# Optimization experiments

Measured on AMD Instinct MI355X. Metric: run time of the kernel, lower is better.

## Reference

```python
import jax, jax.numpy as jnp
import numpy as np
from jax import lax


def _na_indices(size, k):
    # NATTEN-style window: window shifts to stay inside the volume.
    centers = np.arange(size)
    start = np.clip(centers - k // 2, 0, size - k)
    idx = start[:, None] + np.arange(k)[None, :]          # (size, k) neighbor coords
    rel = idx - centers[:, None] + (k - 1)                # (size, k) in [0, 2k-2]
    return jnp.asarray(idx), jnp.asarray(rel)


def _ln(x, g, b):
    mu = jnp.mean(x, axis=-1, keepdims=True)
    var = jnp.mean(jnp.square(x - mu), axis=-1, keepdims=True)
    return (x - mu) * lax.rsqrt(var + 1e-5) * g + b


def setup_inputs() -> dict:
    key = jax.random.key(0)
    ks = jax.random.split(key, 12)
    B, C, H, W, Z = 1, 128, 64, 64, 8
    heads, k = 8, 3
    s = lambda kk, shp: (jax.random.normal(kk, shp, jnp.float32) * 0.02)
    return {
        "x": jax.random.normal(ks[0], (B, C, H, W, Z), jnp.float32),
        "ln1_g": jnp.ones((C,), jnp.float32), "ln1_b": jnp.zeros((C,), jnp.float32),
        "qkv_w": s(ks[1], (C, 3 * C)), "qkv_b": jnp.zeros((3 * C,), jnp.float32),
        "proj_w": s(ks[2], (C, C)), "proj_b": jnp.zeros((C,), jnp.float32),
        "rpb": s(ks[3], (heads, 2 * k - 1, 2 * k - 1, 2 * k - 1)),
        "ln2_g": jnp.ones((C,), jnp.float32), "ln2_b": jnp.zeros((C,), jnp.float32),
        "w1": s(ks[4], (C, 4 * C)), "b1": jnp.zeros((4 * C,), jnp.float32),
        "w2": s(ks[5], (4 * C, C)), "b2": jnp.zeros((C,), jnp.float32),
    }


def reference(x, ln1_g, ln1_b, qkv_w, qkv_b, proj_w, proj_b, rpb,
              ln2_g, ln2_b, w1, b1, w2, b2):
    B, C, H, W, Z = x.shape
    heads = rpb.shape[0]
    k = (rpb.shape[1] + 1) // 2
    hd = C // heads
    K3 = k * k * k

    xp = jnp.transpose(x, (0, 2, 3, 4, 1))                 # (B,H,W,Z,C)
    res1 = xp
    xn = _ln(xp, ln1_g, ln1_b)
    qkv = xn @ qkv_w + qkv_b
    q, kk, v = jnp.split(qkv, 3, axis=-1)

    ih, rh = _na_indices(H, k)
    iw, rw = _na_indices(W, k)
    iz, rz = _na_indices(Z, k)
    Ih = ih[:, None, None, :, None, None]
    Iw = iw[None, :, None, None, :, None]
    Iz = iz[None, None, :, None, None, :]
    # gathered neighborhoods: (B,H,W,Z,k,k,k,C) -> (B,H,W,Z,K3,heads,hd)
    k_n = kk[:, Ih, Iw, Iz, :].reshape(B, H, W, Z, K3, heads, hd)
    v_n = v[:, Ih, Iw, Iz, :].reshape(B, H, W, Z, K3, heads, hd)
    qh = q.reshape(B, H, W, Z, heads, hd) * (hd ** -0.5)

    # scores: (B,H,W,Z,heads,K3)
    scores = jnp.einsum('bxyzne,bxyzmne->bxyznm', qh, k_n)
    bias = rpb[:, rh[:, None, None, :, None, None],
                  rw[None, :, None, None, :, None],
                  rz[None, None, :, None, None, :]]        # (heads,H,W,Z,k,k,k)
    bias = bias.reshape(heads, H, W, Z, K3).transpose(1, 2, 3, 0, 4)
    attn = jax.nn.softmax(scores + bias[None], axis=-1)

    out = jnp.einsum('bxyznm,bxyzmne->bxyzne', attn, v_n).reshape(B, H, W, Z, C)
    out = out @ proj_w + proj_b
    x1 = res1 + out                                        # attention residual
    h = jax.nn.gelu(_ln(x1, ln2_g, ln2_b) @ w1 + b1) @ w2 + b2
    x2 = x1 + h                                            # FFN residual

    enc = jnp.transpose(x2, (0, 4, 1, 2, 3))               # (B,C,H,W,Z)
    skip = enc + x                                         # outer residual
    pooled = lax.reduce_window(skip, -jnp.inf, lax.max,
                               (1, 1, 2, 2, 2), (1, 1, 2, 2, 2), 'VALID')
    return (pooled, skip)
```

## Files before the change

### kernel.cpp

```cpp
#include <hip/hip_runtime.h>
#include <hip/hip_bf16.h>
#include <math.h>

#define NPOS 32768

typedef __hip_bfloat16 bf16;
typedef __attribute__((ext_vector_type(8))) short bf16x8;
typedef __attribute__((ext_vector_type(4))) float f32x4;

__device__ __forceinline__ float bf2f(short s) {
    union { unsigned u; float f; } cv;
    cv.u = ((unsigned)(unsigned short)s) << 16;
    return cv.f;
}

__global__ __launch_bounds__(256) void prep_weights_kernel(
    const float* __restrict__ qkv_w, const float* __restrict__ proj_w,
    const float* __restrict__ w1, const float* __restrict__ w2,
    bf16* __restrict__ wt_qkv, bf16* __restrict__ wt_proj,
    bf16* __restrict__ wt_w1, bf16* __restrict__ wt_w2)
{
    int bi = blockIdx.x;
    const float* src; bf16* dst; int K, M, t;
    if (bi < 48)       { src = qkv_w;  dst = wt_qkv;  K = 128; M = 384; t = bi; }
    else if (bi < 64)  { src = proj_w; dst = wt_proj; K = 128; M = 128; t = bi - 48; }
    else if (bi < 128) { src = w1;     dst = wt_w1;   K = 128; M = 512; t = bi - 64; }
    else               { src = w2;     dst = wt_w2;   K = 512; M = 128; t = bi - 128; }
    int tiles_x = M >> 5;
    int m0 = (t % tiles_x) * 32, k0 = (t / tiles_x) * 32;
    __shared__ float tile[32][33];
    int tx = threadIdx.x & 31, ty = threadIdx.x >> 5;
    #pragma unroll
    for (int i = 0; i < 4; i++)
        tile[ty + i * 8][tx] = src[(size_t)(k0 + ty + i * 8) * M + m0 + tx];
    __syncthreads();
    #pragma unroll
    for (int i = 0; i < 4; i++)
        dst[(size_t)(m0 + ty + i * 8) * K + k0 + tx] = __float2bfloat16(tile[tx][ty + i * 8]);
}

__global__ __launch_bounds__(256) void ln1_transpose_kernel(
    const float* __restrict__ x, const float* __restrict__ g,
    const float* __restrict__ b, bf16* __restrict__ out)
{
    __shared__ float tile[128][65];
    __shared__ float red[2][64][4];
    __shared__ float smu[64], srs[64];
    int n0 = blockIdx.x * 64;
    int tid = threadIdx.x;
    #pragma unroll
    for (int i = 0; i < 32; i++) {
        int idx = i * 256 + tid;
        int c = idx >> 6, nn = idx & 63;
        tile[c][nn] = x[(size_t)c * NPOS + n0 + nn];
    }
    __syncthreads();
    {
        int p = tid >> 2, s = tid & 3;
        float sum = 0.f, ssq = 0.f;
        #pragma unroll
        for (int i = 0; i < 32; i++) {
            float v = tile[s * 32 + i][p];
            sum += v; ssq += v * v;
        }
        red[0][p][s] = sum; red[1][p][s] = ssq;
    }
    __syncthreads();
    if (tid < 64) {
        float s = red[0][tid][0] + red[0][tid][1] + red[0][tid][2] + red[0][tid][3];
        float q = red[1][tid][0] + red[1][tid][1] + red[1][tid][2] + red[1][tid][3];
        float mu = s * (1.f / 128.f);
        float var = q * (1.f / 128.f) - mu * mu;
        smu[tid] = mu;
        srs[tid] = rsqrtf(var + 1e-5f);
    }
    __syncthreads();
    #pragma unroll
    for (int i = 0; i < 32; i++) {
        int idx = i * 256 + tid;
        int nn = idx >> 7, c = idx & 127;
        out[(size_t)(n0 + nn) * 128 + c] =
            __float2bfloat16((tile[c][nn] - smu[nn]) * srs[nn] * g[c] + b[c]);
    }
}

__device__ __forceinline__ float gelu_f(float v) {
    float t = tanhf(0.7978845608028654f * (v + 0.044715f * v * v * v));
    return 0.5f * v * (1.f + t);
}

template<int MODE>
__global__ __launch_bounds__(256) void gemm_mfma_kernel(
    const bf16* __restrict__ A, const bf16* __restrict__ Bt,
    const float* __restrict__ bias, float* __restrict__ outf, bf16* __restrict__ outb,
    const float* __restrict__ aux0, const float* __restrict__ aux1,
    const float* __restrict__ lng, const float* __restrict__ lnb,
    int N, int K, int M)
{
    __shared__ __align__(16) char smem[69632];
    bf16 (*As)[136] = (bf16(*)[136])smem;
    bf16 (*Bs)[136] = (bf16(*)[136])(smem + 34816);

    int tid = threadIdx.x;
    int row0 = blockIdx.x * 128;
    int col0 = blockIdx.y * 128;
    int lane = tid & 63, wid = tid >> 6;
    int wr = wid >> 1, wc = wid & 1;
    int lr = lane & 15, kg = lane >> 4;

    f32x4 acc[4][4] = {};

    for (int k0 = 0; k0 < K; k0 += 128) {
        bf16x8 ra[8], rb[8];
        #pragma unroll
        for (int i = 0; i < 8; i++) {
            int q = i * 256 + tid;
            int r = q >> 4, c16 = q & 15;
            ra[i] = *(const bf16x8*)(A  + (size_t)(row0 + r) * K + k0 + c16 * 8);
            rb[i] = *(const bf16x8*)(Bt + (size_t)(col0 + r) * K + k0 + c16 * 8);
        }
        if (k0 > 0) __syncthreads();
        #pragma unroll
        for (int i = 0; i < 8; i++) {
            int q = i * 256 + tid;
            int r = q >> 4, c16 = q & 15;
            *(bf16x8*)&As[r][c16 * 8] = ra[i];
            *(bf16x8*)&Bs[r][c16 * 8] = rb[i];
        }
        __syncthreads();
        #pragma unroll
        for (int ks = 0; ks < 4; ks++) {
            bf16x8 af[4], bf_[4];
            #pragma unroll
            for (int m = 0; m < 4; m++)
                af[m] = *(const bf16x8*)&As[wr * 64 + m * 16 + lr][ks * 32 + kg * 8];
            #pragma unroll
            for (int n = 0; n < 4; n++)
                bf_[n] = *(const bf16x8*)&Bs[wc * 64 + n * 16 + lr][ks * 32 + kg * 8];
            #pragma unroll
            for (int m = 0; m < 4; m++)
                #pragma unroll
                for (int n = 0; n < 4; n++)
                    acc[m][n] = __builtin_amdgcn_mfma_f32_16x16x32_bf16(af[m], bf_[n], acc[m][n], 0, 0, 0);
        }
    }

    if (MODE == 0 || MODE == 2 || MODE == 3) {
        #pragma unroll
        for (int m = 0; m < 4; m++) {
            #pragma unroll
            for (int n = 0; n < 4; n++) {
                int c = col0 + wc * 64 + n * 16 + lr;
                float bv = bias[c];
                #pragma unroll
                for (int j = 0; j < 4; j++) {
                    int r = row0 + wr * 64 + m * 16 + kg * 4 + j;
                    float v = acc[m][n][j] + bv;
                    if (MODE == 0) {
                        outb[(size_t)r * M + c] = __float2bfloat16(v);
                    } else if (MODE == 2) {
                        outb[(size_t)r * M + c] = __float2bfloat16(gelu_f(v));
                    } else {
                        v += aux1[(size_t)r * 128 + c] + aux0[(size_t)c * N + r];
                        outf[(size_t)c * N + r] = v;
                    }
                }
            }
        }
    } else {
        __syncthreads();
        float (*rsum)[33] = (float(*)[33])smem;
        float (*rsq)[33]  = (float(*)[33])(smem + 16896);
        float* smu = (float*)(smem + 33792);
        float* srs = (float*)(smem + 34304);
        int slot = wc * 16 + lr;
        #pragma unroll
        for (int m = 0; m < 4; m++) {
            #pragma unroll
            for (int j = 0; j < 4; j++) {
                int rloc = wr * 64 + m * 16 + kg * 4 + j;
                int r = row0 + rloc;
                float ps = 0.f, pq = 0.f;
                #pragma unroll
                for (int n = 0; n < 4; n++) {
                    int c = wc * 64 + n * 16 + lr;
                    float v = acc[m][n][j] + bias[c] + aux0[(size_t)c * N + r];
                    acc[m][n][j] = v;
                    outf[(size_t)r * 128 + c] = v;
                    ps += v; pq += v * v;
                }
                rsum[rloc][slot] = ps;
                rsq[rloc][slot]  = pq;
            }
        }
        __syncthreads();
        if (tid < 128) {
            float s = 0.f, q = 0.f;
            #pragma unroll
            for (int i = 0; i < 32; i++) { s += rsum[tid][i]; q += rsq[tid][i]; }
            float mu = s * (1.f / 128.f);
            float var = q * (1.f / 128.f) - mu * mu;
            smu[tid] = mu;
            srs[tid] = rsqrtf(var + 1e-5f);
        }
        __syncthreads();
        #pragma unroll
        for (int m = 0; m < 4; m++) {
            #pragma unroll
            for (int j = 0; j < 4; j++) {
                int rloc = wr * 64 + m * 16 + kg * 4 + j;
                int r = row0 + rloc;
                float mu = smu[rloc], rs = srs[rloc];
                #pragma unroll
                for (int n = 0; n < 4; n++) {
                    int c = wc * 64 + n * 16 + lr;
                    float v = (acc[m][n][j] - mu) * rs * lng[c] + lnb[c];
                    outb[(size_t)r * 128 + c] = __float2bfloat16(v);
                }
            }
        }
    }
}

__global__ __launch_bounds__(256) void attn_kernel(
    const bf16* __restrict__ qkv,
    const float* __restrict__ rpb,
    bf16* __restrict__ out)
{
    int t = blockIdx.x * 256 + threadIdx.x;
    int head = t & 7, n = t >> 3;
    int z = n & 7, w = (n >> 3) & 63, h = n >> 9;

    int sh = min(max(h - 1, 0), 61);
    int sw = min(max(w - 1, 0), 61);
    int sz = min(max(z - 1, 0), 5);

    float qf[16];
    {
        const bf16* qp = qkv + (size_t)n * 384 + head * 16;
        bf16x8 q0 = *(const bf16x8*)qp;
        bf16x8 q1 = *(const bf16x8*)(qp + 8);
        #pragma unroll
        for (int e = 0; e < 8; e++) {
            qf[e]     = bf2f(q0[e]) * 0.25f;
            qf[e + 8] = bf2f(q1[e]) * 0.25f;
        }
    }

    const bf16*  kbase = qkv + (size_t)((sh << 9) + (sw << 3) + sz) * 384 + 128 + head * 16;
    const float* rp    = rpb + head * 125 + (sh - h + 2) * 25 + (sw - w + 2) * 5 + (sz - z + 2);

    float sc[27];
    float mx = -1e30f;
    #pragma unroll
    for (int a = 0; a < 3; a++) {
        #pragma unroll
        for (int b = 0; b < 3; b++) {
            #pragma unroll
            for (int c = 0; c < 3; c++) {
                const bf16* kp = kbase + (size_t)(a * 512 + b * 8 + c) * 384;
                bf16x8 k0 = *(const bf16x8*)kp;
                bf16x8 k1 = *(const bf16x8*)(kp + 8);
                float s = 0.f;
                #pragma unroll
                for (int e = 0; e < 8; e++) s = fmaf(qf[e], bf2f(k0[e]), s);
                #pragma unroll
                for (int e = 0; e < 8; e++) s = fmaf(qf[e + 8], bf2f(k1[e]), s);
                s += rp[a * 25 + b * 5 + c];
                sc[a * 9 + b * 3 + c] = s;
                mx = fmaxf(mx, s);
            }
        }
    }

    float sum = 0.f;
    #pragma unroll
    for (int m = 0; m < 27; m++) {
        float e = __expf(sc[m] - mx);
        sc[m] = e;
        sum += e;
    }
    float inv = 1.f / sum;

    float o[16] = {};
    #pragma unroll
    for (int a = 0; a < 3; a++) {
        #pragma unroll
        for (int b = 0; b < 3; b++) {
            #pragma unroll
            for (int c = 0; c < 3; c++) {
                const bf16* vp = kbase + (size_t)(a * 512 + b * 8 + c) * 384 + 128;
                bf16x8 v0 = *(const bf16x8*)vp;
                bf16x8 v1 = *(const bf16x8*)(vp + 8);
                float pm = sc[a * 9 + b * 3 + c];
                #pragma unroll
                for (int e = 0; e < 8; e++) {
                    o[e]     = fmaf(pm, bf2f(v0[e]), o[e]);
                    o[e + 8] = fmaf(pm, bf2f(v1[e]), o[e + 8]);
                }
            }
        }
    }

    short os[16];
    #pragma unroll
    for (int e = 0; e < 16; e++) {
        union { bf16 b; short s; } cv;
        cv.b = __float2bfloat16(o[e] * inv);
        os[e] = cv.s;
    }
    bf16* op = out + (size_t)n * 128 + head * 16;
    *(bf16x8*)op       = *(bf16x8*)os;
    *(bf16x8*)(op + 8) = *(bf16x8*)(os + 8);
}

__global__ __launch_bounds__(256) void pool_kernel(
    const float* __restrict__ skip, float* __restrict__ pooled)
{
    int t = blockIdx.x * 256 + threadIdx.x;
    if (t >= 128 * 32 * 32 * 4) return;
    int oz = t & 3, ow = (t >> 2) & 31, oh = (t >> 7) & 31, c = t >> 12;
    const float* base = skip + (size_t)c * 32768 + (oh * 2) * 512 + (ow * 2) * 8 + oz * 2;
    float m = -INFINITY;
    #pragma unroll
    for (int dh = 0; dh < 2; dh++)
        #pragma unroll
        for (int dw = 0; dw < 2; dw++)
            #pragma unroll
            for (int dz = 0; dz < 2; dz++)
                m = fmaxf(m, base[dh * 512 + dw * 8 + dz]);
    pooled[t] = m;
}

extern "C" void kernel_launch(void* const* d_in, const int* in_sizes, int n_in,
                              void* d_out, int out_size, void* d_ws, size_t ws_size,
                              hipStream_t stream) {
    const float* x      = (const float*)d_in[0];
    const float* ln1_g  = (const float*)d_in[1];
    const float* ln1_b  = (const float*)d_in[2];
    const float* qkv_w  = (const float*)d_in[3];
    const float* qkv_b  = (const float*)d_in[4];
    const float* proj_w = (const float*)d_in[5];
    const float* proj_b = (const float*)d_in[6];
    const float* rpb    = (const float*)d_in[7];
    const float* ln2_g  = (const float*)d_in[8];
    const float* ln2_b  = (const float*)d_in[9];
    const float* w1     = (const float*)d_in[10];
    const float* b1     = (const float*)d_in[11];
    const float* w2     = (const float*)d_in[12];
    const float* b2     = (const float*)d_in[13];

    const int N = NPOS;
    char* wsc = (char*)d_ws;
    bf16*  buf0 = (bf16*)wsc;
    bf16*  buf1 = (bf16*)(wsc + (size_t)N * 128 * 2);
    float* buf2 = (float*)(wsc + (size_t)N * 128 * 2 + (size_t)N * 512 * 2);
    char*  wts  = wsc + (size_t)N * 128 * 2 + (size_t)N * 512 * 2 + (size_t)N * 128 * 4;
    bf16* wt_qkv  = (bf16*)wts;
    bf16* wt_proj = wt_qkv  + 384 * 128;
    bf16* wt_w1   = wt_proj + 128 * 128;
    bf16* wt_w2   = wt_w1   + 512 * 128;

    float* out_pooled = (float*)d_out;
    float* out_skip   = (float*)d_out + 524288;

    prep_weights_kernel<<<192, 256, 0, stream>>>(qkv_w, proj_w, w1, w2,
                                                 wt_qkv, wt_proj, wt_w1, wt_w2);

    ln1_transpose_kernel<<<N / 64, 256, 0, stream>>>(x, ln1_g, ln1_b, buf0);

    gemm_mfma_kernel<0><<<dim3(N / 128, 3), 256, 0, stream>>>(
        buf0, wt_qkv, qkv_b, nullptr, buf1, nullptr, nullptr, nullptr, nullptr, N, 128, 384);

    attn_kernel<<<(N * 8) / 256, 256, 0, stream>>>(buf1, rpb, buf0);

    gemm_mfma_kernel<4><<<dim3(N / 128, 1), 256, 0, stream>>>(
        buf0, wt_proj, proj_b, buf2, buf0, x, nullptr, ln2_g, ln2_b, N, 128, 128);

    gemm_mfma_kernel<2><<<dim3(N / 128, 4), 256, 0, stream>>>(
        buf0, wt_w1, b1, nullptr, buf1, nullptr, nullptr, nullptr, nullptr, N, 128, 512);

    gemm_mfma_kernel<3><<<dim3(N / 128, 1), 256, 0, stream>>>(
        buf1, wt_w2, b2, out_skip, nullptr, x, buf2, nullptr, nullptr, N, 512, 128);

    pool_kernel<<<(524288 + 255) / 256, 256, 0, stream>>>(out_skip, out_pooled);
}
```

Measured before the change: 209.1 us.

## Drop LDS staging in GEMMs, load MFMA fragments directly, shrink row tiles

The GEMM kernel no longer stages A and B tiles through shared memory. Each wave loads its MFMA fragments straight from global memory, and the K loop is fully unrolled through a compile-time K template. The projection and W2 GEMMs now use 64-row tiles, which doubles their block count and improves occupancy. GELU is rewritten as a sigmoid form using __expf instead of tanhf. The direct loads give up LDS reuse across waves, so global and L2 traffic go up, and register pressure rises from the fully unrolled loop.

Result: no change. 209.6 us (+0.2%).

```diff
diff --git a/kernel.cpp b/kernel.cpp
--- a/kernel.cpp
+++ b/kernel.cpp
@@ -85,76 +85,57 @@
 }
 
 __device__ __forceinline__ float gelu_f(float v) {
-    float t = tanhf(0.7978845608028654f * (v + 0.044715f * v * v * v));
-    return 0.5f * v * (1.f + t);
-}
-
-template<int MODE>
+    float u = 0.7978845608028654f * (v + 0.044715f * v * v * v);
+    return v / (1.f + __expf(-2.f * u));
+}
+
+template<int MODE, int BM, int KT>
 __global__ __launch_bounds__(256) void gemm_mfma_kernel(
     const bf16* __restrict__ A, const bf16* __restrict__ Bt,
     const float* __restrict__ bias, float* __restrict__ outf, bf16* __restrict__ outb,
     const float* __restrict__ aux0, const float* __restrict__ aux1,
     const float* __restrict__ lng, const float* __restrict__ lnb,
-    int N, int K, int M)
-{
-    __shared__ __align__(16) char smem[69632];
-    bf16 (*As)[136] = (bf16(*)[136])smem;
-    bf16 (*Bs)[136] = (bf16(*)[136])(smem + 34816);
-
+    int N, int M)
+{
+    constexpr int MF = BM / 32;
     int tid = threadIdx.x;
-    int row0 = blockIdx.x * 128;
+    int row0 = blockIdx.x * BM;
     int col0 = blockIdx.y * 128;
     int lane = tid & 63, wid = tid >> 6;
     int wr = wid >> 1, wc = wid & 1;
     int lr = lane & 15, kg = lane >> 4;
 
-    f32x4 acc[4][4] = {};
-
-    for (int k0 = 0; k0 < K; k0 += 128) {
-        bf16x8 ra[8], rb[8];
-        #pragma unroll
-        for (int i = 0; i < 8; i++) {
-            int q = i * 256 + tid;
-            int r = q >> 4, c16 = q & 15;
-            ra[i] = *(const bf16x8*)(A  + (size_t)(row0 + r) * K + k0 + c16 * 8);
-            rb[i] = *(const bf16x8*)(Bt + (size_t)(col0 + r) * K + k0 + c16 * 8);
-        }
-        if (k0 > 0) __syncthreads();
-        #pragma unroll
-        for (int i = 0; i < 8; i++) {
-            int q = i * 256 + tid;
-            int r = q >> 4, c16 = q & 15;
-            *(bf16x8*)&As[r][c16 * 8] = ra[i];
-            *(bf16x8*)&Bs[r][c16 * 8] = rb[i];
-        }
-        __syncthreads();
-        #pragma unroll
-        for (int ks = 0; ks < 4; ks++) {
-            bf16x8 af[4], bf_[4];
-            #pragma unroll
-            for (int m = 0; m < 4; m++)
-                af[m] = *(const bf16x8*)&As[wr * 64 + m * 16 + lr][ks * 32 + kg * 8];
+    const bf16* Ap = A  + (size_t)(row0 + wr * (BM / 2) + lr) * KT + kg * 8;
+    const bf16* Bp = Bt + (size_t)(col0 + wc * 64 + lr) * KT + kg * 8;
+
+    f32x4 acc[MF][4] = {};
+
+    #pragma unroll
+    for (int k0 = 0; k0 < KT; k0 += 32) {
+        bf16x8 af[MF], bf_[4];
+        #pragma unroll
+        for (int m = 0; m < MF; m++)
+            af[m] = *(const bf16x8*)(Ap + (size_t)(m * 16) * KT + k0);
+        #pragma unroll
+        for (int n = 0; n < 4; n++)
+            bf_[n] = *(const bf16x8*)(Bp + (size_t)(n * 16) * KT + k0);
+        #pragma unroll
+        for (int m = 0; m < MF; m++)
             #pragma unroll
             for (int n = 0; n < 4; n++)
-                bf_[n] = *(const bf16x8*)&Bs[wc * 64 + n * 16 + lr][ks * 32 + kg * 8];
-            #pragma unroll
-            for (int m = 0; m < 4; m++)
-                #pragma unroll
-                for (int n = 0; n < 4; n++)
-                    acc[m][n] = __builtin_amdgcn_mfma_f32_16x16x32_bf16(af[m], bf_[n], acc[m][n], 0, 0, 0);
-        }
+                acc[m][n] = __builtin_amdgcn_mfma_f32_16x16x32_bf16(af[m], bf_[n], acc[m][n], 0, 0, 0);
     }
 
     if (MODE == 0 || MODE == 2 || MODE == 3) {
         #pragma unroll
-        for (int m = 0; m < 4; m++) {
+        for (int m = 0; m < MF; m++) {
             #pragma unroll
             for (int n = 0; n < 4; n++) {
                 int c = col0 + wc * 64 + n * 16 + lr;
                 float bv = bias[c];
                 #pragma unroll
                 for (int j = 0; j < 4; j++) {
-                    int r = row0 + wr * 64 + m * 16 + kg * 4 + j;
+                    int r = row0 + wr * (BM / 2) + m * 16 + kg * 4 + j;
                     float v = acc[m][n][j] + bv;
                     if (MODE == 0) {
                         outb[(size_t)r * M + c] = __float2bfloat16(v);
@@ -168,17 +149,15 @@
             }
         }
     } else {
-        __syncthreads();
-        float (*rsum)[33] = (float(*)[33])smem;
-        float (*rsq)[33]  = (float(*)[33])(smem + 16896);
-        float* smu = (float*)(smem + 33792);
-        float* srs = (float*)(smem + 34304);
+        __shared__ float rsum[64][33];
+        __shared__ float rsq[64][33];
+        __shared__ float smu[64], srs[64];
         int slot = wc * 16 + lr;
         #pragma unroll
-        for (int m = 0; m < 4; m++) {
+        for (int m = 0; m < MF; m++) {
             #pragma unroll
             for (int j = 0; j < 4; j++) {
-                int rloc = wr * 64 + m * 16 + kg * 4 + j;
+                int rloc = wr * (BM / 2) + m * 16 + kg * 4 + j;
                 int r = row0 + rloc;
                 float ps = 0.f, pq = 0.f;
                 #pragma unroll
@@ -194,7 +173,7 @@
             }
         }
         __syncthreads();
-        if (tid < 128) {
+        if (tid < 64) {
             float s = 0.f, q = 0.f;
             #pragma unroll
             for (int i = 0; i < 32; i++) { s += rsum[tid][i]; q += rsq[tid][i]; }
@@ -205,10 +184,10 @@
         }
         __syncthreads();
         #pragma unroll
-        for (int m = 0; m < 4; m++) {
+        for (int m = 0; m < MF; m++) {
             #pragma unroll
             for (int j = 0; j < 4; j++) {
-                int rloc = wr * 64 + m * 16 + kg * 4 + j;
+                int rloc = wr * (BM / 2) + m * 16 + kg * 4 + j;
                 int r = row0 + rloc;
                 float mu = smu[rloc], rs = srs[rloc];
                 #pragma unroll
@@ -369,19 +348,19 @@
 
     ln1_transpose_kernel<<<N / 64, 256, 0, stream>>>(x, ln1_g, ln1_b, buf0);
 
-    gemm_mfma_kernel<0><<<dim3(N / 128, 3), 256, 0, stream>>>(
-        buf0, wt_qkv, qkv_b, nullptr, buf1, nullptr, nullptr, nullptr, nullptr, N, 128, 384);
+    gemm_mfma_kernel<0, 128, 128><<<dim3(N / 128, 3), 256, 0, stream>>>(
+        buf0, wt_qkv, qkv_b, nullptr, buf1, nullptr, nullptr, nullptr, nullptr, N, 384);
 
     attn_kernel<<<(N * 8) / 256, 256, 0, stream>>>(buf1, rpb, buf0);
 
-    gemm_mfma_kernel<4><<<dim3(N / 128, 1), 256, 0, stream>>>(
-        buf0, wt_proj, proj_b, buf2, buf0, x, nullptr, ln2_g, ln2_b, N, 128, 128);
-
-    gemm_mfma_kernel<2><<<dim3(N / 128, 4), 256, 0, stream>>>(
-        buf0, wt_w1, b1, nullptr, buf1, nullptr, nullptr, nullptr, nullptr, N, 128, 512);
-
-    gemm_mfma_kernel<3><<<dim3(N / 128, 1), 256, 0, stream>>>(
-        buf1, wt_w2, b2, out_skip, nullptr, x, buf2, nullptr, nullptr, N, 512, 128);
+    gemm_mfma_kernel<4, 64, 128><<<dim3(N / 64, 1), 256, 0, stream>>>(
+        buf0, wt_proj, proj_b, buf2, buf0, x, nullptr, ln2_g, ln2_b, N, 128);
+
+    gemm_mfma_kernel<2, 128, 128><<<dim3(N / 128, 4), 256, 0, stream>>>(
+        buf0, wt_w1, b1, nullptr, buf1, nullptr, nullptr, nullptr, nullptr, N, 512);
+
+    gemm_mfma_kernel<3, 64, 512><<<dim3(N / 64, 1), 256, 0, stream>>>(
+        buf1, wt_w2, b2, out_skip, nullptr, x, buf2, nullptr, nullptr, N, 128);
 
     pool_kernel<<<(524288 + 255) / 256, 256, 0, stream>>>(out_skip, out_pooled);
 }
```
